# Performance work log

Measured on AMD Instinct MI355X. Metric: run time of the kernel, lower is better.

The kernel has to match this reference:

```python
import jax, jax.numpy as jnp
import numpy as np

B, T, D = 32, 4096, 256
LN_EPS = 1e-5


def setup_inputs() -> dict:
    key = jax.random.key(0)
    k0, k1, k2 = jax.random.split(key, 3)
    byte_ids = jax.random.randint(k0, (B, T), 0, 256, dtype=jnp.int32)
    freq_bands = jnp.ones((D // 2,), jnp.float32)  # nn.Parameter(torch.ones(embed_dim//2))
    # freq_proj: Linear(D, 2D) -> LayerNorm(2D) -> GELU -> Linear(2D, D)
    w1 = jax.random.normal(k1, (D, 2 * D), jnp.float32) * (1.0 / np.sqrt(D))
    b1 = jnp.zeros((2 * D,), jnp.float32)
    gamma = jnp.ones((2 * D,), jnp.float32)
    beta = jnp.zeros((2 * D,), jnp.float32)
    w2 = jax.random.normal(k2, (2 * D, D), jnp.float32) * (1.0 / np.sqrt(2 * D))
    b2 = jnp.zeros((D,), jnp.float32)
    return dict(byte_ids=byte_ids, freq_bands=freq_bands, w1=w1, b1=b1,
                gamma=gamma, beta=beta, w2=w2, b2=b2)


def reference(byte_ids, freq_bands, w1, b1, gamma, beta, w2, b2):
    Bsz, Tlen = byte_ids.shape
    Dm = w1.shape[0]
    k = min(Dm // 2, Tlen // 2)  # static
    signal = byte_ids.astype(jnp.float32) / 127.5 - 1.0  # [B,T]
    # Single FFT; FFT(roll(signal, -pos))[f] == X[f] * exp(+2i*pi*f*pos/T),
    # so |spectrum| is position-invariant and angle shifts linearly in pos.
    X = jnp.fft.fft(signal, axis=1)[:, :k]           # [B,k] complex64
    mag = jnp.abs(X) * freq_bands[:k]                 # [B,k]
    phase0 = jnp.angle(X)                             # [B,k]
    pos = jnp.arange(Tlen, dtype=jnp.float32)
    f = jnp.arange(k, dtype=jnp.float32)
    shift = (2.0 * np.pi / Tlen) * pos[:, None] * f[None, :]      # [T,k]
    phase = phase0[:, None, :] + shift[None, :, :]                 # [B,T,k]
    mag_bt = jnp.broadcast_to(mag[:, None, :], (Bsz, Tlen, k))     # [B,T,k]
    feats = jnp.concatenate([mag_bt, jnp.sin(phase), jnp.cos(phase)], axis=-1)  # [B,T,3k]
    if feats.shape[-1] < Dm:
        feats = jnp.pad(feats, ((0, 0), (0, 0), (0, Dm - feats.shape[-1])))
    else:
        feats = feats[..., :Dm]                        # truncate (drops cos tail)
    # freq_proj MLP
    h = feats @ w1 + b1                                # [B,T,2D]
    mu = jnp.mean(h, axis=-1, keepdims=True)
    var = jnp.var(h, axis=-1, keepdims=True)
    h = (h - mu) * jax.lax.rsqrt(var + LN_EPS) * gamma + beta
    h = jax.nn.gelu(h, approximate=False)              # torch nn.GELU default = exact erf
    return h @ w2 + b2                                 # [B,T,D]
```

## Files before the change

kernel.cpp:

```cpp
#include <hip/hip_runtime.h>


#define T_SZ   4096
#define NFREQ  128

typedef short    bf16x8 __attribute__((ext_vector_type(8)));
typedef unsigned u32x4  __attribute__((ext_vector_type(4)));
typedef float    f32x4  __attribute__((ext_vector_type(4)));

__device__ __forceinline__ float bf2f(unsigned short x) {
  union { unsigned u; float f; } v; v.u = ((unsigned)x) << 16; return v.f;
}
__device__ __forceinline__ float bits2f(unsigned u) {
  union { unsigned u; float f; } v; v.u = u; return v.f;
}
__device__ __forceinline__ unsigned short f2bf(float x) {
  union { float f; unsigned u; } v; v.f = x;
  unsigned r = v.u + 0x7fffu + ((v.u >> 16) & 1u);
  return (unsigned short)(r >> 16);
}
__device__ __forceinline__ unsigned pk2(float lo, float hi) {
  union { float f; unsigned u; } a, b;
  a.f = lo; b.f = hi;
  return __builtin_amdgcn_perm(b.u + 0x8000u, a.u + 0x8000u, 0x07060302u);
}
__device__ __forceinline__ bf16x8 as_bf(u32x4 v) { return __builtin_bit_cast(bf16x8, v); }
__device__ __forceinline__ bool probe_f32(const unsigned* p) {
  return p[0] == 0x3F800000u;
}
__device__ __forceinline__ void stage16(const void* g, const void* lds_base) {
  __builtin_amdgcn_global_load_lds(
      (const __attribute__((address_space(1))) unsigned int*)g,
      (__attribute__((address_space(3))) unsigned int*)lds_base, 16, 0, 0);
}
__device__ __forceinline__ float gelu_f(float v) {
  float u = v * (0.7978845608f + 0.0356774081f * v * v);
  float d = 1.0f + exp2f(-2.885390082f * u);
  return v * __builtin_amdgcn_rcpf(d);
}

__global__ void dft_part_kernel(const int* __restrict__ ids,
                                float2* __restrict__ part) {
  int bid = blockIdx.x;
  int b  = bid >> 6;
  int fg = (bid >> 3) & 7;
  int tp = bid & 7;
  int fl = threadIdx.x >> 4;
  int m  = threadIdx.x & 15;
  int f  = fg * 16 + fl;
  const int* row = ids + b * T_SZ + tp * 512;
  const float C = 6.283185307179586f / 4096.0f;
  float re = 0.f, im = 0.f;
  #pragma unroll
  for (int i = 0; i < 8; ++i) {
    int t0 = i * 64 + m * 4;
    int4 iv = *(const int4*)(row + t0);
    int a = ((tp * 512 + t0) * f) & 4095;
#define DFT1(VAL) { float s = (float)(VAL) * (1.0f / 127.5f) - 1.0f;          \
                    float ang = (float)a * C;                                 \
                    re += s * __cosf(ang); im -= s * __sinf(ang);             \
                    a = (a + f) & 4095; }
    DFT1(iv.x) DFT1(iv.y) DFT1(iv.z) DFT1(iv.w)
#undef DFT1
  }
  #pragma unroll
  for (int mask = 1; mask < 16; mask <<= 1) {
    re += __shfl_xor(re, mask, 64);
    im += __shfl_xor(im, mask, 64);
  }
  if (m == 0) part[(tp * 32 + b) * 128 + f] = make_float2(re, im);
}

__global__ void prep1_kernel(const void* __restrict__ w1, const void* __restrict__ w2,
                             const void* __restrict__ gamma, const void* __restrict__ beta,
                             const void* __restrict__ b2, const void* __restrict__ fb,
                             const float2* __restrict__ part,
                             unsigned short* __restrict__ mag,
                             float* __restrict__ ph0,
                             unsigned short* __restrict__ w1sin,
                             unsigned short* __restrict__ w2tp,
                             unsigned short* __restrict__ bia) {
  bool f32 = probe_f32((const unsigned*)fb);
  int bid = blockIdx.x, tid = threadIdx.x;
  if (bid < 16) {
    int idx = bid * 256 + tid;
    int b = idx >> 7, f = idx & 127;
    float re = 0.f, im = 0.f;
    #pragma unroll
    for (int p = 0; p < 8; ++p) {
      float2 v = part[(p * 32 + b) * 128 + f];
      re += v.x; im += v.y;
    }
    float fbv = f32 ? ((const float*)fb)[f] : bf2f(((const unsigned short*)fb)[f]);
    mag[b * NFREQ + f] = f2bf(sqrtf(re * re + im * im) * fbv);
    ph0[b * NFREQ + f] = atan2f(im, re);
  } else if (bid < 272) {
    int o = (bid - 16) * 256 + tid;
    int f = o & 127, n1 = o >> 7;
    int idx = (128 + f) * 512 + n1;
    w1sin[o] = f32 ? f2bf(((const float*)w1)[idx]) : ((const unsigned short*)w1)[idx];
  } else if (bid < 784) {
    int o = (bid - 272) * 256 + tid;
    int p = o & 511, n2 = o >> 9;
    int n1 = ((p >> 5) << 5) | (((p >> 2) & 1) << 4) | (((p >> 3) & 3) << 2) | (p & 3);
    int idx = n1 * 256 + n2;
    w2tp[o] = f32 ? f2bf(((const float*)w2)[idx]) : ((const unsigned short*)w2)[idx];
  } else {
    int i = (bid - 784) * 256 + tid;
    const void* src; int off;
    if (i < 512)       { src = gamma; off = i; }
    else if (i < 1024) { src = beta;  off = i - 512; }
    else               { src = b2;    off = i - 1024; }
    bia[i] = f32 ? f2bf(((const float*)src)[off]) : ((const unsigned short*)src)[off];
  }
}

__global__ void hmag_kernel(const void* __restrict__ w1, const void* __restrict__ b1,
                            const unsigned* __restrict__ probe,
                            const unsigned short* __restrict__ mag,
                            float* __restrict__ hmag) {
  __shared__ float red[256];
  bool f32 = probe_f32(probe);
  int bid = blockIdx.x;
  int b = bid >> 3, n1g = bid & 7;
  int tid = threadIdx.x;
  int fq = tid >> 6, n1l = tid & 63;
  int n1 = n1g * 64 + n1l;
  const unsigned short* mrow = mag + b * NFREQ;
  float acc = 0.f;
  for (int f = fq * 32; f < fq * 32 + 32; ++f) {
    float wv = f32 ? ((const float*)w1)[f * 512 + n1]
                   : bf2f(((const unsigned short*)w1)[f * 512 + n1]);
    acc += bf2f(mrow[f]) * bf2f(f2bf(wv));
  }
  red[tid] = acc;
  __syncthreads();
  if (tid < 64) {
    int n1o = n1g * 64 + tid;
    float a = red[tid] + red[64 + tid] + red[128 + tid] + red[192 + tid];
    float bv = f32 ? ((const float*)b1)[n1o] : bf2f(((const unsigned short*)b1)[n1o]);
    hmag[b * 512 + n1o] = a + bv;
  }
}

__global__ __launch_bounds__(256, 2)
void fused_kernel(const unsigned short* __restrict__ w1sin,
                  const unsigned short* __restrict__ w2tp,
                  const unsigned short* __restrict__ bias,
                  const float* __restrict__ hmag,
                  const float* __restrict__ ph0,
                  float* __restrict__ out) {
  __shared__ __align__(16) short lds_w[16384];

  const int tid  = threadIdx.x;
  const int wave = tid >> 6;
  const int lane = tid & 63;
  const int quad = lane >> 4;
  const int col  = lane & 15;

  const int blk  = blockIdx.x;
  const int b    = blk >> 5;
  const int my_t = ((blk & 31) << 6) + (wave << 4) + col;

  {
    short* bufp = lds_w;
    #pragma unroll
    for (int i = 0; i < 4; ++i) {
      int rl = wave * 16 + i * 4 + quad;
      int gch = (lane & 15) ^ (rl & 15);
      stage16(w1sin + ((0 * 64 + rl) * 128 + gch * 8), bufp + (wave * 16 + i * 4) * 128);
    }
  }

  u32x4 BsA[4], BsB[4];
  const float* php = ph0 + b * NFREQ;
  const float PHC = 6.283185307179586f / 4096.0f;
  #pragma unroll
  for (int s = 0; s < 4; ++s) {
    u32x4 awA, awB;
    #pragma unroll
    for (int w = 0; w < 4; ++w) {
      int f0 = s * 32 + quad * 8 + w * 2;
      float a0 = __sinf(php[f0]     + (float)((my_t * f0) & 4095) * PHC);
      float a1 = __sinf(php[f0 + 1] + (float)((my_t * (f0 + 1)) & 4095) * PHC);
      awA[w] = pk2(a0, a1);
      awB[w] = awA[w] ^ 0x80000000u;
    }
    BsA[s] = awA; BsB[s] = awB;
  }

  __syncthreads();

  const float* hmagb = hmag + b * 512;
  u32x4 B2A[16], B2B[16];
  float sumA = 0.f, ssqA = 0.f, sumB = 0.f, ssqB = 0.f;
  #pragma unroll
  for (int h = 0; h < 8; ++h) {
    short* cur = lds_w + (h & 1) * 8192;
    short* nxt = lds_w + ((h + 1) & 1) * 8192;
    if (h < 7) {
      #pragma unroll
      for (int i = 0; i < 4; ++i) {
        int rl = wave * 16 + i * 4 + quad;
        int gch = (lane & 15) ^ (rl & 15);
        stage16(w1sin + (((h + 1) * 64 + rl) * 128 + gch * 8),
                nxt + (wave * 16 + i * 4) * 128);
      }
    } else {
      #pragma unroll
      for (int i = 0; i < 4; ++i) {
        int rl = i * 4 + wave;
        int gch = lane ^ (rl & 15);
        stage16(w2tp + ((0 * 16 + rl) * 512 + gch * 8), nxt + rl * 512);
      }
    }
    f32x4 pA = {0.f, 0.f, 0.f, 0.f}, pB = {0.f, 0.f, 0.f, 0.f};
    #pragma unroll
    for (int ntl = 0; ntl < 4; ++ntl) {
      f32x4 aA = *(const f32x4*)(hmagb + h * 64 + ntl * 16 + 4 * quad);
      f32x4 aB = aA;
      #pragma unroll
      for (int s = 0; s < 4; ++s) {
        bf16x8 frag = *(const bf16x8*)(cur + (ntl * 16 + col) * 128
                                           + (((s * 4 + quad) ^ col) << 3));
        aA = __builtin_amdgcn_mfma_f32_16x16x32_bf16(frag, as_bf(BsA[s]), aA, 0, 0, 0);
        aB = __builtin_amdgcn_mfma_f32_16x16x32_bf16(frag, as_bf(BsB[s]), aB, 0, 0, 0);
      }
      #pragma unroll
      for (int jj = 0; jj < 4; ++jj) {
        sumA += aA[jj]; ssqA += aA[jj] * aA[jj];
        sumB += aB[jj]; ssqB += aB[jj] * aB[jj];
      }
      if ((ntl & 1) == 0) { pA = aA; pB = aB; }
      else {
        int s2l = h * 2 + (ntl >> 1);
        u32x4 hA, hB;
        hA[0] = pk2(pA[0], pA[1]); hA[1] = pk2(pA[2], pA[3]);
        hA[2] = pk2(aA[0], aA[1]); hA[3] = pk2(aA[2], aA[3]);
        hB[0] = pk2(pB[0], pB[1]); hB[1] = pk2(pB[2], pB[3]);
        hB[2] = pk2(aB[0], aB[1]); hB[3] = pk2(aB[2], aB[3]);
        B2A[s2l] = hA;
        B2B[s2l] = hB;
      }
    }
    __syncthreads();
  }

  sumA += __shfl_xor(sumA, 16, 64); sumA += __shfl_xor(sumA, 32, 64);
  ssqA += __shfl_xor(ssqA, 16, 64); ssqA += __shfl_xor(ssqA, 32, 64);
  sumB += __shfl_xor(sumB, 16, 64); sumB += __shfl_xor(sumB, 32, 64);
  ssqB += __shfl_xor(ssqB, 16, 64); ssqB += __shfl_xor(ssqB, 32, 64);
  float muA = sumA * (1.0f / 512.0f);
  float varA = fmaxf(ssqA * (1.0f / 512.0f) - muA * muA, 0.0f);
  float rsA = rsqrtf(varA + 1e-5f);
  float muB = sumB * (1.0f / 512.0f);
  float varB = fmaxf(ssqB * (1.0f / 512.0f) - muB * muB, 0.0f);
  float rsB = rsqrtf(varB + 1e-5f);

  const unsigned short* gptr  = bias;
  const unsigned short* beptr = bias + 512;
  #pragma unroll
  for (int s2 = 0; s2 < 16; ++s2) {
    u32x4 hwA = B2A[s2], hwB = B2B[s2], owA, owB;
    #pragma unroll
    for (int w = 0; w < 4; ++w) {
      int nt  = 2 * s2 + (w >> 1);
      int n1b = nt * 16 + 4 * quad + (w & 1) * 2;
      unsigned gp = *(const unsigned*)(gptr + n1b);
      unsigned bp = *(const unsigned*)(beptr + n1b);
      float g0 = bits2f(gp << 16),  g1 = bits2f(gp & 0xffff0000u);
      float e0 = bits2f(bp << 16),  e1 = bits2f(bp & 0xffff0000u);
      float hA0 = bits2f(hwA[w] << 16), hA1 = bits2f(hwA[w] & 0xffff0000u);
      float hB0 = bits2f(hwB[w] << 16), hB1 = bits2f(hwB[w] & 0xffff0000u);
      float tA0 = rsA * g0, tA1 = rsA * g1;
      float tB0 = rsB * g0, tB1 = rsB * g1;
      float vA0 = fmaf(hA0, tA0, fmaf(-muA, tA0, e0));
      float vA1 = fmaf(hA1, tA1, fmaf(-muA, tA1, e1));
      float vB0 = fmaf(hB0, tB0, fmaf(-muB, tB0, e0));
      float vB1 = fmaf(hB1, tB1, fmaf(-muB, tB1, e1));
      owA[w] = pk2(gelu_f(vA0), gelu_f(vA1));
      owB[w] = pk2(gelu_f(vB0), gelu_f(vB1));
    }
    B2A[s2] = owA;
    B2B[s2] = owB;
  }

  const unsigned short* b2p = bias + 1024;
  const long orowA = (long)(b * T_SZ + my_t) * 256;
  const long orowB = orowA + (long)2048 * 256;
  #pragma unroll
  for (int h = 0; h < 16; ++h) {
    short* cur = lds_w + (h & 1) * 8192;
    short* nxt = lds_w + ((h + 1) & 1) * 8192;
    if (h < 15) {
      #pragma unroll
      for (int i = 0; i < 4; ++i) {
        int rl = i * 4 + wave;
        int gch = lane ^ (rl & 15);
        stage16(w2tp + (((h + 1) * 16 + rl) * 512 + gch * 8), nxt + rl * 512);
      }
    }
    unsigned bp0 = *(const unsigned*)(b2p + h * 16 + 4 * quad);
    unsigned bp1 = *(const unsigned*)(b2p + h * 16 + 4 * quad + 2);
    f32x4 ccA0 = { bits2f(bp0 << 16), bits2f(bp0 & 0xffff0000u),
                   bits2f(bp1 << 16), bits2f(bp1 & 0xffff0000u) };
    f32x4 ccB0 = ccA0;
    f32x4 ccA1 = {0.f, 0.f, 0.f, 0.f};
    f32x4 ccB1 = {0.f, 0.f, 0.f, 0.f};
    #pragma unroll
    for (int s2 = 0; s2 < 16; s2 += 2) {
      bf16x8 A2a = *(const bf16x8*)(cur + col * 512 + (((s2 * 4 + quad) ^ col) << 3));
      bf16x8 A2b = *(const bf16x8*)(cur + col * 512 + ((((s2 + 1) * 4 + quad) ^ col) << 3));
      ccA0 = __builtin_amdgcn_mfma_f32_16x16x32_bf16(A2a, as_bf(B2A[s2]),     ccA0, 0, 0, 0);
      ccB0 = __builtin_amdgcn_mfma_f32_16x16x32_bf16(A2a, as_bf(B2B[s2]),     ccB0, 0, 0, 0);
      ccA1 = __builtin_amdgcn_mfma_f32_16x16x32_bf16(A2b, as_bf(B2A[s2 + 1]), ccA1, 0, 0, 0);
      ccB1 = __builtin_amdgcn_mfma_f32_16x16x32_bf16(A2b, as_bf(B2B[s2 + 1]), ccB1, 0, 0, 0);
    }
    f32x4 ccA = ccA0 + ccA1;
    f32x4 ccB = ccB0 + ccB1;
    *(f32x4*)(out + orowA + h * 16 + quad * 4) = ccA;
    *(f32x4*)(out + orowB + h * 16 + quad * 4) = ccB;
    if (h < 15) __syncthreads();
  }
}

extern "C" void kernel_launch(void* const* d_in, const int* in_sizes, int n_in,
                              void* d_out, int out_size, void* d_ws, size_t ws_size,
                              hipStream_t stream) {
  const int*      ids   = (const int*)d_in[0];
  const void*     fb    = d_in[1];
  const void*     w1    = d_in[2];
  const void*     b1    = d_in[3];
  const void*     gamma = d_in[4];
  const void*     beta  = d_in[5];
  const void*     w2    = d_in[6];
  const void*     b2    = d_in[7];
  float*          out   = (float*)d_out;
  const unsigned* probe = (const unsigned*)fb;

  char* ws = (char*)d_ws;
  unsigned short* mag   = (unsigned short*)(ws);
  float*          ph0   = (float*)(ws + 8192);
  unsigned short* bia   = (unsigned short*)(ws + 24576);
  float*          hmag  = (float*)(ws + 32768);
  unsigned short* w1sin = (unsigned short*)(ws + 98304);
  unsigned short* w2tp  = (unsigned short*)(ws + 229376);
  float2*         part  = (float2*)(ws + 491520);

  dft_part_kernel<<<dim3(2048), dim3(256), 0, stream>>>(ids, part);
  prep1_kernel<<<dim3(789), dim3(256), 0, stream>>>(w1, w2, gamma, beta, b2, fb,
                                                    part, mag, ph0, w1sin, w2tp, bia);
  hmag_kernel<<<dim3(256), dim3(256), 0, stream>>>(w1, b1, probe, mag, hmag);
  fused_kernel<<<dim3(1024), dim3(256), 0, stream>>>(w1sin, w2tp, bia, hmag, ph0, out);
}
```

Baseline: 244.1 us.

## Merge prep kernels into two launches and simplify second-GEMM accumulation chain

Folds the DFT partial-sum kernel and the weight conversion/transposition work into one launch, and merges the magnitude/phase finalisation with the hmag projection into a second launch. Each hmag block now recomputes its row's magnitudes into shared memory instead of reading them from a workspace buffer, which drops one launch and one global round trip. The second GEMM loop in the fused kernel goes back to a single accumulator pair per output, which lengthens the MFMA dependency chain but frees registers.

```diff
diff --git a/kernel.cpp b/kernel.cpp
--- a/kernel.cpp
+++ b/kernel.cpp
@@ -39,74 +39,60 @@
   return v * __builtin_amdgcn_rcpf(d);
 }
 
-__global__ void dft_part_kernel(const int* __restrict__ ids,
-                                float2* __restrict__ part) {
-  int bid = blockIdx.x;
-  int b  = bid >> 6;
-  int fg = (bid >> 3) & 7;
-  int tp = bid & 7;
-  int fl = threadIdx.x >> 4;
-  int m  = threadIdx.x & 15;
-  int f  = fg * 16 + fl;
-  const int* row = ids + b * T_SZ + tp * 512;
-  const float C = 6.283185307179586f / 4096.0f;
-  float re = 0.f, im = 0.f;
-  #pragma unroll
-  for (int i = 0; i < 8; ++i) {
-    int t0 = i * 64 + m * 4;
-    int4 iv = *(const int4*)(row + t0);
-    int a = ((tp * 512 + t0) * f) & 4095;
+__global__ void combo1_kernel(const int* __restrict__ ids,
+                              const void* __restrict__ w1, const void* __restrict__ w2,
+                              const void* __restrict__ gamma, const void* __restrict__ beta,
+                              const void* __restrict__ b2, const void* __restrict__ fb,
+                              float2* __restrict__ part,
+                              unsigned short* __restrict__ w1sin,
+                              unsigned short* __restrict__ w2tp,
+                              unsigned short* __restrict__ bia) {
+  int bid = blockIdx.x, tid = threadIdx.x;
+  if (bid < 2048) {
+    int b  = bid >> 6;
+    int fg = (bid >> 3) & 7;
+    int tp = bid & 7;
+    int fl = tid >> 4;
+    int m  = tid & 15;
+    int f  = fg * 16 + fl;
+    const int* row = ids + b * T_SZ + tp * 512;
+    const float C = 6.283185307179586f / 4096.0f;
+    float re = 0.f, im = 0.f;
+    #pragma unroll
+    for (int i = 0; i < 8; ++i) {
+      int t0 = i * 64 + m * 4;
+      int4 iv = *(const int4*)(row + t0);
+      int a = ((tp * 512 + t0) * f) & 4095;
 #define DFT1(VAL) { float s = (float)(VAL) * (1.0f / 127.5f) - 1.0f;          \
                     float ang = (float)a * C;                                 \
                     re += s * __cosf(ang); im -= s * __sinf(ang);             \
                     a = (a + f) & 4095; }
-    DFT1(iv.x) DFT1(iv.y) DFT1(iv.z) DFT1(iv.w)
+      DFT1(iv.x) DFT1(iv.y) DFT1(iv.z) DFT1(iv.w)
 #undef DFT1
-  }
-  #pragma unroll
-  for (int mask = 1; mask < 16; mask <<= 1) {
-    re += __shfl_xor(re, mask, 64);
-    im += __shfl_xor(im, mask, 64);
-  }
-  if (m == 0) part[(tp * 32 + b) * 128 + f] = make_float2(re, im);
-}
-
-__global__ void prep1_kernel(const void* __restrict__ w1, const void* __restrict__ w2,
-                             const void* __restrict__ gamma, const void* __restrict__ beta,
-                             const void* __restrict__ b2, const void* __restrict__ fb,
-                             const float2* __restrict__ part,
-                             unsigned short* __restrict__ mag,
-                             float* __restrict__ ph0,
-                             unsigned short* __restrict__ w1sin,
-                             unsigned short* __restrict__ w2tp,
-                             unsigned short* __restrict__ bia) {
+    }
+    #pragma unroll
+    for (int mask = 1; mask < 16; mask <<= 1) {
+      re += __shfl_xor(re, mask, 64);
+      im += __shfl_xor(im, mask, 64);
+    }
+    if (m == 0) part[(tp * 32 + b) * 128 + f] = make_float2(re, im);
+    return;
+  }
   bool f32 = probe_f32((const unsigned*)fb);
-  int bid = blockIdx.x, tid = threadIdx.x;
-  if (bid < 16) {
-    int idx = bid * 256 + tid;
-    int b = idx >> 7, f = idx & 127;
-    float re = 0.f, im = 0.f;
-    #pragma unroll
-    for (int p = 0; p < 8; ++p) {
-      float2 v = part[(p * 32 + b) * 128 + f];
-      re += v.x; im += v.y;
-    }
-    float fbv = f32 ? ((const float*)fb)[f] : bf2f(((const unsigned short*)fb)[f]);
-    mag[b * NFREQ + f] = f2bf(sqrtf(re * re + im * im) * fbv);
-    ph0[b * NFREQ + f] = atan2f(im, re);
-  } else if (bid < 272) {
-    int o = (bid - 16) * 256 + tid;
+  int id2 = bid - 2048;
+  if (id2 < 256) {
+    int o = id2 * 256 + tid;
     int f = o & 127, n1 = o >> 7;
     int idx = (128 + f) * 512 + n1;
     w1sin[o] = f32 ? f2bf(((const float*)w1)[idx]) : ((const unsigned short*)w1)[idx];
-  } else if (bid < 784) {
-    int o = (bid - 272) * 256 + tid;
+  } else if (id2 < 768) {
+    int o = (id2 - 256) * 256 + tid;
     int p = o & 511, n2 = o >> 9;
     int n1 = ((p >> 5) << 5) | (((p >> 2) & 1) << 4) | (((p >> 3) & 3) << 2) | (p & 3);
     int idx = n1 * 256 + n2;
     w2tp[o] = f32 ? f2bf(((const float*)w2)[idx]) : ((const unsigned short*)w2)[idx];
   } else {
-    int i = (bid - 784) * 256 + tid;
+    int i = (id2 - 768) * 256 + tid;
     const void* src; int off;
     if (i < 512)       { src = gamma; off = i; }
     else if (i < 1024) { src = beta;  off = i - 512; }
@@ -115,29 +101,53 @@
   }
 }
 
-__global__ void hmag_kernel(const void* __restrict__ w1, const void* __restrict__ b1,
-                            const unsigned* __restrict__ probe,
-                            const unsigned short* __restrict__ mag,
-                            float* __restrict__ hmag) {
-  __shared__ float red[256];
-  bool f32 = probe_f32(probe);
-  int bid = blockIdx.x;
-  int b = bid >> 3, n1g = bid & 7;
-  int tid = threadIdx.x;
+__global__ void combo2_kernel(const void* __restrict__ w1, const void* __restrict__ b1,
+                              const void* __restrict__ fb,
+                              const float2* __restrict__ part,
+                              float* __restrict__ ph0,
+                              float* __restrict__ hmag) {
+  __shared__ float smem[384];
+  int bid = blockIdx.x, tid = threadIdx.x;
+  bool f32 = probe_f32((const unsigned*)fb);
+  if (bid < 16) {
+    int idx = bid * 256 + tid;
+    int b = idx >> 7, f = idx & 127;
+    float re = 0.f, im = 0.f;
+    #pragma unroll
+    for (int p = 0; p < 8; ++p) {
+      float2 v = part[(p * 32 + b) * 128 + f];
+      re += v.x; im += v.y;
+    }
+    ph0[b * NFREQ + f] = atan2f(im, re);
+    return;
+  }
+  int bid2 = bid - 16;
+  int b = bid2 >> 3, n1g = bid2 & 7;
+  if (tid < 128) {
+    int f = tid;
+    float re = 0.f, im = 0.f;
+    #pragma unroll
+    for (int p = 0; p < 8; ++p) {
+      float2 v = part[(p * 32 + b) * 128 + f];
+      re += v.x; im += v.y;
+    }
+    float fbv = f32 ? ((const float*)fb)[f] : bf2f(((const unsigned short*)fb)[f]);
+    smem[f] = bf2f(f2bf(sqrtf(re * re + im * im) * fbv));
+  }
+  __syncthreads();
   int fq = tid >> 6, n1l = tid & 63;
   int n1 = n1g * 64 + n1l;
-  const unsigned short* mrow = mag + b * NFREQ;
   float acc = 0.f;
   for (int f = fq * 32; f < fq * 32 + 32; ++f) {
     float wv = f32 ? ((const float*)w1)[f * 512 + n1]
                    : bf2f(((const unsigned short*)w1)[f * 512 + n1]);
-    acc += bf2f(mrow[f]) * bf2f(f2bf(wv));
-  }
-  red[tid] = acc;
+    acc += smem[f] * bf2f(f2bf(wv));
+  }
+  smem[128 + tid] = acc;
   __syncthreads();
   if (tid < 64) {
     int n1o = n1g * 64 + tid;
-    float a = red[tid] + red[64 + tid] + red[128 + tid] + red[192 + tid];
+    float a = smem[128 + tid] + smem[192 + tid] + smem[256 + tid] + smem[320 + tid];
     float bv = f32 ? ((const float*)b1)[n1o] : bf2f(((const unsigned short*)b1)[n1o]);
     hmag[b * 512 + n1o] = a + bv;
   }
@@ -302,22 +312,15 @@
     }
     unsigned bp0 = *(const unsigned*)(b2p + h * 16 + 4 * quad);
     unsigned bp1 = *(const unsigned*)(b2p + h * 16 + 4 * quad + 2);
-    f32x4 ccA0 = { bits2f(bp0 << 16), bits2f(bp0 & 0xffff0000u),
-                   bits2f(bp1 << 16), bits2f(bp1 & 0xffff0000u) };
-    f32x4 ccB0 = ccA0;
-    f32x4 ccA1 = {0.f, 0.f, 0.f, 0.f};
-    f32x4 ccB1 = {0.f, 0.f, 0.f, 0.f};
-    #pragma unroll
-    for (int s2 = 0; s2 < 16; s2 += 2) {
-      bf16x8 A2a = *(const bf16x8*)(cur + col * 512 + (((s2 * 4 + quad) ^ col) << 3));
-      bf16x8 A2b = *(const bf16x8*)(cur + col * 512 + ((((s2 + 1) * 4 + quad) ^ col) << 3));
-      ccA0 = __builtin_amdgcn_mfma_f32_16x16x32_bf16(A2a, as_bf(B2A[s2]),     ccA0, 0, 0, 0);
-      ccB0 = __builtin_amdgcn_mfma_f32_16x16x32_bf16(A2a, as_bf(B2B[s2]),     ccB0, 0, 0, 0);
-      ccA1 = __builtin_amdgcn_mfma_f32_16x16x32_bf16(A2b, as_bf(B2A[s2 + 1]), ccA1, 0, 0, 0);
-      ccB1 = __builtin_amdgcn_mfma_f32_16x16x32_bf16(A2b, as_bf(B2B[s2 + 1]), ccB1, 0, 0, 0);
-    }
-    f32x4 ccA = ccA0 + ccA1;
-    f32x4 ccB = ccB0 + ccB1;
+    f32x4 ccA = { bits2f(bp0 << 16), bits2f(bp0 & 0xffff0000u),
+                  bits2f(bp1 << 16), bits2f(bp1 & 0xffff0000u) };
+    f32x4 ccB = ccA;
+    #pragma unroll
+    for (int s2 = 0; s2 < 16; ++s2) {
+      bf16x8 A2 = *(const bf16x8*)(cur + col * 512 + (((s2 * 4 + quad) ^ col) << 3));
+      ccA = __builtin_amdgcn_mfma_f32_16x16x32_bf16(A2, as_bf(B2A[s2]), ccA, 0, 0, 0);
+      ccB = __builtin_amdgcn_mfma_f32_16x16x32_bf16(A2, as_bf(B2B[s2]), ccB, 0, 0, 0);
+    }
     *(f32x4*)(out + orowA + h * 16 + quad * 4) = ccA;
     *(f32x4*)(out + orowB + h * 16 + quad * 4) = ccB;
     if (h < 15) __syncthreads();
@@ -336,10 +339,8 @@
   const void*     w2    = d_in[6];
   const void*     b2    = d_in[7];
   float*          out   = (float*)d_out;
-  const unsigned* probe = (const unsigned*)fb;
 
   char* ws = (char*)d_ws;
-  unsigned short* mag   = (unsigned short*)(ws);
   float*          ph0   = (float*)(ws + 8192);
   unsigned short* bia   = (unsigned short*)(ws + 24576);
   float*          hmag  = (float*)(ws + 32768);
@@ -347,9 +348,8 @@
   unsigned short* w2tp  = (unsigned short*)(ws + 229376);
   float2*         part  = (float2*)(ws + 491520);
 
-  dft_part_kernel<<<dim3(2048), dim3(256), 0, stream>>>(ids, part);
-  prep1_kernel<<<dim3(789), dim3(256), 0, stream>>>(w1, w2, gamma, beta, b2, fb,
-                                                    part, mag, ph0, w1sin, w2tp, bia);
-  hmag_kernel<<<dim3(256), dim3(256), 0, stream>>>(w1, b1, probe, mag, hmag);
+  combo1_kernel<<<dim3(2821), dim3(256), 0, stream>>>(ids, w1, w2, gamma, beta, b2, fb,
+                                                      part, w1sin, w2tp, bia);
+  combo2_kernel<<<dim3(272), dim3(256), 0, stream>>>(w1, b1, fb, part, ph0, hmag);
   fused_kernel<<<dim3(1024), dim3(256), 0, stream>>>(w1sin, w2tp, bia, hmag, ph0, out);
 }
```

Measured after the change: 231.9 us. -5.0%, faster.
